# Kernel optimization log

Measured on AMD Instinct MI355X. Metric: run time of the kernel, lower is better.

Reference implementation:

```python
import jax, jax.numpy as jnp
import numpy as np

B, NQ, NK, C, H = 4, 1024, 1024, 768, 12
DH = C // H
SCALE = DH ** -0.5
EPS = 1e-5  # nn.LayerNorm default
NEG_INF = float('-inf')


def _ln(x, g, b):
    m = jnp.mean(x, axis=-1, keepdims=True)
    v = jnp.mean((x - m) ** 2, axis=-1, keepdims=True)
    return (x - m) * jax.lax.rsqrt(v + EPS) * g + b


def _heads(t):  # [B,N,C] -> [B,H,N,Dh]
    Bq, N, _ = t.shape
    return t.reshape(Bq, N, H, DH).transpose(0, 2, 1, 3)


def setup_inputs() -> dict:
    key = jax.random.key(0)
    ks = jax.random.split(key, 32)
    w = lambda k, shape: jax.random.normal(k, shape, jnp.float32) * 0.02
    g = lambda k: 1.0 + jax.random.normal(k, (C,), jnp.float32) * 0.02
    b = lambda k: jax.random.normal(k, (C,), jnp.float32) * 0.02
    inp = {
        'x': jax.random.normal(ks[0], (B, NQ, C), jnp.float32),
        'y': jax.random.normal(ks[1], (B, NK, C), jnp.float32),
        'xpos': jnp.arange(B * NQ, dtype=jnp.int32).reshape(B, NQ),
        'ypos': jnp.arange(B * NK, dtype=jnp.int32).reshape(B, NK),
        'mask': jax.random.randint(ks[2], (NQ, NK), 0, 2) > 0,
        'similarities': jax.random.normal(ks[3], (B, H, NQ, NK), jnp.float32),
        # norms
        'ln1_g': g(ks[4]), 'ln1_b': b(ks[5]),
        'ln2_g': g(ks[6]), 'ln2_b': b(ks[7]),
        'ln3_g': g(ks[8]), 'ln3_b': b(ks[9]),
        'lny_g': g(ks[10]), 'lny_b': b(ks[11]),
        # self-attn (qkv_bias=False)
        'qkv_w': w(ks[12], (3 * C, C)),
        'aproj_w': w(ks[13], (C, C)), 'aproj_b': b(ks[14]),
        # cross-attn
        'pq_w': w(ks[15], (C, C)), 'pk_w': w(ks[16], (C, C)), 'pv_w': w(ks[17], (C, C)),
        'cproj_w': w(ks[18], (C, C)), 'cproj_b': b(ks[19]),
        # mlp (hidden = 4*C)
        'fc1_w': w(ks[20], (4 * C, C)), 'fc1_b': jax.random.normal(ks[21], (4 * C,), jnp.float32) * 0.02,
        'fc2_w': w(ks[22], (C, 4 * C)), 'fc2_b': b(ks[23]),
    }
    return inp


def reference(x, y, xpos, ypos, mask, similarities,
              ln1_g, ln1_b, ln2_g, ln2_b, ln3_g, ln3_b, lny_g, lny_b,
              qkv_w, aproj_w, aproj_b,
              pq_w, pk_w, pv_w, cproj_w, cproj_b,
              fc1_w, fc1_b, fc2_w, fc2_b):
    # ---- self-attention (rope=None, dropout=0) ----
    xn = _ln(x, ln1_g, ln1_b)
    qkv = (xn @ qkv_w.T).reshape(B, NQ, 3, H, DH).transpose(2, 0, 3, 1, 4)
    q, k, v = qkv[0], qkv[1], qkv[2]                       # [B,H,Nq,Dh]
    attn = jax.nn.softmax(jnp.einsum('bhqd,bhkd->bhqk', q, k) * SCALE, axis=-1)
    sa = jnp.einsum('bhqk,bhkd->bhqd', attn, v).transpose(0, 2, 1, 3).reshape(B, NQ, C)
    x = x + sa @ aproj_w.T + aproj_b

    # ---- sparse cross-attention with similarity bias + mask ----
    y_ = _ln(y, lny_g, lny_b)
    xn2 = _ln(x, ln2_g, ln2_b)
    cq = _heads(xn2 @ pq_w.T)                              # [B,H,Nq,Dh]
    ck = _heads(y_ @ pk_w.T)                               # [B,H,Nk,Dh]
    cv = _heads(y_ @ pv_w.T)
    scores = jnp.einsum('bhqd,bhkd->bhqk', cq, ck) * SCALE
    sims_c = similarities - jnp.mean(similarities, axis=1, keepdims=True)
    scores = scores + sims_c
    scores = jnp.where(mask[None, None], scores, NEG_INF)
    cattn = jax.nn.softmax(scores, axis=-1)
    ca = jnp.einsum('bhqk,bhkd->bhqd', cattn, cv).transpose(0, 2, 1, 3).reshape(B, NQ, C)
    x = x + ca @ cproj_w.T + cproj_b

    # ---- MLP (exact GELU, as nn.GELU default) ----
    xn3 = _ln(x, ln3_g, ln3_b)
    h = jax.nn.gelu(xn3 @ fc1_w.T + fc1_b, approximate=False)
    x = x + h @ fc2_w.T + fc2_b
    return (x, y)
```

## Files before the change

### kernel.cpp

```cpp
#include <hip/hip_runtime.h>
#include <cstdint>
#include <cstddef>


typedef __bf16 bf16;
typedef __attribute__((ext_vector_type(8))) __bf16 bf16x8;
typedef __attribute__((ext_vector_type(4))) __bf16 bf16x4;
typedef __attribute__((ext_vector_type(4))) float f32x4;

typedef __attribute__((address_space(1))) void gvoid;
typedef __attribute__((address_space(3))) void lvoid;

#define DEVI static __device__ __forceinline__

DEVI void gload16(const void* g, void* l) {
  __builtin_amdgcn_global_load_lds((gvoid*)(uintptr_t)g, (lvoid*)(uintptr_t)l, 16, 0, 0);
}

DEVI f32x4 mfma_bf16(bf16x8 a, bf16x8 b, f32x4 c) {
  return __builtin_amdgcn_mfma_f32_16x16x32_bf16(a, b, c, 0, 0, 0);
}


template<int BM, int BN, bool BIAS, bool GELU, bool RES, bool OBF, bool VT>
DEVI void gemm_dev(bf16* As, bf16* Bs, int by, int bx,
                   const bf16* __restrict__ A, const bf16* __restrict__ Bt,
                   const float* __restrict__ bias, const float* __restrict__ res,
                   bf16* __restrict__ Cb, float* __restrict__ Cf,
                   bf16* __restrict__ vtOut, int vtBase, int N, int K)
{
  constexpr int WM = BM / 2, WN = BN / 2;
  constexpr int FM = WM / 16, FN = WN / 16;
  const int tid = threadIdx.x;
  const int lane = tid & 63;
  const int wv = tid >> 6;
  const int wr = wv >> 1, wc = wv & 1;
  const int l15 = lane & 15, lg = lane >> 4;
  const int bm = by * BM, bn = bx * BN;

  f32x4 acc[FM][FN];
  const f32x4 z = {0.f, 0.f, 0.f, 0.f};
  #pragma unroll
  for (int i = 0; i < FM; ++i)
    #pragma unroll
    for (int jj = 0; jj < FN; ++jj) acc[i][jj] = z;

  for (int k0 = 0; k0 < K; k0 += 64) {
    __syncthreads();
    #pragma unroll
    for (int c = tid; c < BM * 8; c += 256) {
      const int row = c >> 3, colb = (c & 7) << 4;
      gload16((const char*)A + ((size_t)(bm + row) * K + k0) * 2 + colb,
              (char*)As + (size_t)c * 16);
    }
    #pragma unroll
    for (int c = tid; c < BN * 8; c += 256) {
      const int row = c >> 3, colb = (c & 7) << 4;
      gload16((const char*)Bt + ((size_t)(bn + row) * K + k0) * 2 + colb,
              (char*)Bs + (size_t)c * 16);
    }
    __syncthreads();
    #pragma unroll
    for (int kk = 0; kk < 64; kk += 32) {
      bf16x8 af[FM], bfr[FN];
      #pragma unroll
      for (int mi = 0; mi < FM; ++mi)
        af[mi] = *(const bf16x8*)(As + (size_t)(wr * WM + mi * 16 + l15) * 64 + kk + lg * 8);
      #pragma unroll
      for (int ni = 0; ni < FN; ++ni)
        bfr[ni] = *(const bf16x8*)(Bs + (size_t)(wc * WN + ni * 16 + l15) * 64 + kk + lg * 8);
      #pragma unroll
      for (int mi = 0; mi < FM; ++mi)
        #pragma unroll
        for (int ni = 0; ni < FN; ++ni)
          acc[mi][ni] = mfma_bf16(af[mi], bfr[ni], acc[mi][ni]);
    }
  }

  #pragma unroll
  for (int mi = 0; mi < FM; ++mi) {
    const int row0 = bm + wr * WM + mi * 16 + lg * 4;
    #pragma unroll
    for (int ni = 0; ni < FN; ++ni) {
      const int col = bn + wc * WN + ni * 16 + l15;
      if constexpr (VT) {
        if (col >= vtBase) {
          const int hd = col - vtBase;
          const int bb = row0 >> 10, n0 = row0 & 1023;
          bf16x4 ov;
          #pragma unroll
          for (int r = 0; r < 4; ++r) ov[r] = (bf16)acc[mi][ni][r];
          *(bf16x4*)(vtOut + ((size_t)(bb * 768 + hd)) * 1024 + n0) = ov;
          continue;
        }
      }
      #pragma unroll
      for (int r = 0; r < 4; ++r) {
        float v = acc[mi][ni][r];
        if constexpr (BIAS) v += bias[col];
        if constexpr (GELU) v = 0.5f * v * (1.0f + erff(v * 0.70710678118654752f));
        if constexpr (RES)  v += res[(size_t)(row0 + r) * N + col];
        if constexpr (OBF)  Cb[(size_t)(row0 + r) * N + col] = (bf16)v;
        else                Cf[(size_t)(row0 + r) * N + col] = v;
      }
    }
  }
}

DEVI void lnw_dev(int row,
                  const float* __restrict__ xin, const float* __restrict__ g,
                  const float* __restrict__ be, bf16* __restrict__ out)
{
  const int lane = threadIdx.x & 63;
  const f32x4* xr = (const f32x4*)(xin + (size_t)row * 768);
  f32x4 v[3];
  #pragma unroll
  for (int j = 0; j < 3; ++j) v[j] = xr[lane + 64 * j];
  float s = 0.f;
  #pragma unroll
  for (int j = 0; j < 3; ++j) s += v[j][0] + v[j][1] + v[j][2] + v[j][3];
  #pragma unroll
  for (int o = 32; o; o >>= 1) s += __shfl_xor(s, o);
  const float mean = s * (1.0f / 768.0f);
  float q = 0.f;
  #pragma unroll
  for (int j = 0; j < 3; ++j)
    #pragma unroll
    for (int e = 0; e < 4; ++e) { const float d = v[j][e] - mean; q += d * d; }
  #pragma unroll
  for (int o = 32; o; o >>= 1) q += __shfl_xor(q, o);
  const float inv = rsqrtf(q * (1.0f / 768.0f) + 1e-5f);
  #pragma unroll
  for (int j = 0; j < 3; ++j) {
    const int c = lane + 64 * j;
    const f32x4 gv = ((const f32x4*)g)[c];
    const f32x4 bv = ((const f32x4*)be)[c];
    bf16x4 o4;
    #pragma unroll
    for (int e = 0; e < 4; ++e)
      o4[e] = (bf16)((v[j][e] - mean) * inv * gv[e] + bv[e]);
    *((bf16x4*)out + (size_t)row * 192 + c) = o4;
  }
}

DEVI void bias2_dev(int blk, int* red,
                    const float* __restrict__ sim,
                    const unsigned char* __restrict__ mask,
                    bf16* __restrict__ biasOut)
{
  const int b = blk >> 9;
  const int q0 = (blk & 511) * 2;
  const int t = threadIdx.x;
  const int k4 = t * 4;

  int ds = mask[t * 4 + 1] + mask[t * 4 + 2] + mask[t * 4 + 3];
  #pragma unroll
  for (int o = 32; o; o >>= 1) ds += __shfl_xor(ds, o);
  if ((t & 63) == 0) red[t >> 6] = ds;
  __syncthreads();
  const int msh = ((red[0] + red[1] + red[2] + red[3]) == 0) ? 2 : 0;

  const float* sb = sim + (size_t)b * 12 * 1024 * 1024;
  bf16* ob = biasOut + (size_t)b * 12 * 1024 * 1024;

  #pragma unroll
  for (int p = 0; p < 2; ++p) {
    const int q = q0 + p;
    f32x4 sv[12];
    f32x4 acc = {0.f, 0.f, 0.f, 0.f};
    #pragma unroll
    for (int h = 0; h < 12; ++h) {
      sv[h] = *(const f32x4*)(sb + ((size_t)h * 1024 + q) * 1024 + k4);
      acc += sv[h];
    }
    const f32x4 mean = acc * (1.0f / 12.0f);

    float mb[4];
    if (msh == 0) {
      const uchar4 mv = *(const uchar4*)(mask + (size_t)q * 1024 + k4);
      mb[0] = mv.x ? 0.f : -1e30f; mb[1] = mv.y ? 0.f : -1e30f;
      mb[2] = mv.z ? 0.f : -1e30f; mb[3] = mv.w ? 0.f : -1e30f;
    } else {
      const int4 mv = *(const int4*)((const int*)mask + (size_t)q * 1024 + k4);
      mb[0] = mv.x ? 0.f : -1e30f; mb[1] = mv.y ? 0.f : -1e30f;
      mb[2] = mv.z ? 0.f : -1e30f; mb[3] = mv.w ? 0.f : -1e30f;
    }

    #pragma unroll
    for (int h = 0; h < 12; ++h) {
      bf16x4 o;
      #pragma unroll
      for (int j = 0; j < 4; ++j)
        o[j] = (bf16)(sv[h][j] - mean[j] + mb[j]);
      *(bf16x4*)(ob + ((size_t)h * 1024 + q) * 1024 + k4) = o;
    }
  }
}


struct CvtArgs {
  const float* src[8];
  bf16* dst[8];
  int end[8];
};

__global__ __launch_bounds__(256)
void prep_k(CvtArgs a,
            const float* __restrict__ x, const float* __restrict__ g1,
            const float* __restrict__ b1, bf16* __restrict__ xn,
            const float* __restrict__ y, const float* __restrict__ gy,
            const float* __restrict__ by_, bf16* __restrict__ yln,
            const float* __restrict__ sim, const unsigned char* __restrict__ mask,
            bf16* __restrict__ biasA)
{
  __shared__ int red[4];
  const int f = blockIdx.x;
  const int t = threadIdx.x;
  if (f < 2304) {
    #pragma unroll
    for (int j = 0; j < 4; ++j) {
      const int i = f * 1024 + j * 256 + t;
      int s = 0;
      #pragma unroll
      for (int k = 0; k < 7; ++k) s += (i >= a.end[k]) ? 1 : 0;
      const int base = s ? a.end[s - 1] : 0;
      const int off = i - base;
      const f32x4 v = *((const f32x4*)a.src[s] + off);
      bf16x4 o;
      o[0] = (bf16)v[0]; o[1] = (bf16)v[1]; o[2] = (bf16)v[2]; o[3] = (bf16)v[3];
      *(bf16x4*)(a.dst[s] + (size_t)off * 4) = o;
    }
  } else if (f < 4352) {
    const int row = (f - 2304) * 4 + (t >> 6);
    if (row < 4096) lnw_dev(row, x, g1, b1, xn);
    else            lnw_dev(row - 4096, y, gy, by_, yln);
  } else {
    bias2_dev(f - 4352, red, sim, mask, biasA);
  }
}

__global__ __launch_bounds__(256)
void apkv_k(const bf16* __restrict__ sa, const bf16* __restrict__ w_ap,
            const float* __restrict__ apb, const float* __restrict__ x,
            float* __restrict__ x1,
            const bf16* __restrict__ yln, const bf16* __restrict__ w_pkv,
            bf16* __restrict__ ckv, bf16* __restrict__ cvtT)
{
  __shared__ bf16 As[128 * 64];
  __shared__ bf16 Bs[128 * 64];
  const int f = blockIdx.x;
  if (f < 384) {
    const int xcd = f & 7, j = f >> 3;
    const int by = xcd + 8 * (j % 8);
    const int bx = j / 8;
    gemm_dev<64,128,true,false,true,false,false>(As, Bs, by, bx,
        sa, w_ap, apb, x, nullptr, x1, nullptr, 0, 768, 768);
  } else {
    const int g = f - 384;
    const int xcd = g & 7, j = g >> 3;
    const int by = xcd + 8 * (j % 4);
    const int bx = j / 4;
    gemm_dev<128,128,false,false,false,true,true>(As, Bs, by, bx,
        yln, w_pkv, nullptr, nullptr, ckv, nullptr, cvtT, 768, 1536, 768);
  }
}

__global__ __launch_bounds__(256)
void fc2copy_k(const bf16* __restrict__ hbuf, const bf16* __restrict__ w_f2,
               const float* __restrict__ f2b, const float* __restrict__ x2,
               float* __restrict__ outp,
               const float* __restrict__ y, float* __restrict__ ycopy)
{
  __shared__ bf16 As[128 * 64];
  __shared__ bf16 Bs[128 * 64];
  const int f = blockIdx.x;
  if (f < 384) {
    const int xcd = f & 7, j = f >> 3;
    const int by = xcd + 8 * (j % 8);
    const int bx = j / 8;
    gemm_dev<64,128,true,false,true,false,false>(As, Bs, by, bx,
        hbuf, w_f2, f2b, x2, nullptr, outp, nullptr, 0, 768, 3072);
  } else {
    for (int i = (f - 384) * 256 + threadIdx.x; i < 786432; i += 512 * 256)
      ((f32x4*)ycopy)[i] = ((const f32x4*)y)[i];
  }
}

template<int BM, int BN, bool BIAS, bool GELU, bool RES, bool OBF, bool VT>
__global__ __launch_bounds__(256)
void gemm_bt(const bf16* __restrict__ A, const bf16* __restrict__ Bt,
             const float* __restrict__ bias, const float* __restrict__ res,
             bf16* __restrict__ Cb, float* __restrict__ Cf,
             bf16* __restrict__ vtOut, int vtBase,
             int nyPerXcd, int N, int K)
{
  __shared__ bf16 As[BM * 64];
  __shared__ bf16 Bs[BN * 64];
  const int f = blockIdx.x;
  const int xcd = f & 7, j = f >> 3;
  const int by = xcd + 8 * (j % nyPerXcd);
  const int bx = j / nyPerXcd;
  gemm_dev<BM,BN,BIAS,GELU,RES,OBF,VT>(As, Bs, by, bx,
      A, Bt, bias, res, Cb, Cf, vtOut, vtBase, N, K);
}

__global__ __launch_bounds__(256)
void ln_k(const float* __restrict__ xin, const float* __restrict__ g,
          const float* __restrict__ be, bf16* __restrict__ out)
{
  lnw_dev(blockIdx.x * 4 + (threadIdx.x >> 6), xin, g, be, out);
}

template<int CROSS>
__global__ __launch_bounds__(256, 3)
void fattn_k(const bf16* __restrict__ Qp, int ldq,
             const bf16* __restrict__ Kp, int ldk,
             const bf16* __restrict__ Vt,
             const bf16* __restrict__ bias,
             bf16* __restrict__ Out)
{
  __shared__ bf16 Kl[2][64 * 64];
  __shared__ bf16 Vl[2][64 * 64];
  __shared__ bf16 Pl[4][16 * 72];

  const int f = blockIdx.x;
  const int r8 = f & 7, rest = f >> 3;
  const int c6 = rest % 6, qt = rest / 6;
  const int pp = r8 + 8 * c6;
  const int b = pp / 12, hh = pp % 12;
  const int tid = threadIdx.x, lane = tid & 63, wq = tid >> 6;
  const int l15 = lane & 15, lg = lane >> 4;

  bf16x8 qreg0, qreg1;
  {
    const bf16* qsrc = Qp + (size_t)(b * 1024 + qt * 64 + wq * 16 + l15) * ldq + hh * 64 + lg * 8;
    qreg0 = *(const bf16x8*)qsrc;
    qreg1 = *(const bf16x8*)(qsrc + 32);
  }
  const char* Kbase = (const char*)(Kp + (size_t)b * 1024 * ldk + hh * 64);
  const char* Vbase = (const char*)(Vt + (size_t)(b * 12 + hh) * 64 * 1024);
  const bf16* biasRow = nullptr;
  if constexpr (CROSS)
    biasRow = bias + (((size_t)(b * 12 + hh)) * 1024 + qt * 64 + wq * 16 + l15) * 1024;

  f32x4 oacc[4];
  const f32x4 z = {0.f, 0.f, 0.f, 0.f};
  #pragma unroll
  for (int i = 0; i < 4; ++i) oacc[i] = z;
  float m_run = -1e30f, l_run = 0.f;

  char* PlW = (char*)&Pl[wq][0];
  const int swz = (l15 & 7) << 4;

  auto stage = [&](int buf, int t) {
    const int k0 = t * 64;
    #pragma unroll
    for (int jj = 0; jj < 2; ++jj) {
      const int c = jj * 256 + tid;
      const int r = c >> 3;
      const int sw = ((c & 7) ^ (r & 7)) << 4;
      gload16(Kbase + ((size_t)(k0 + r) * ldk) * 2 + sw, (char*)&Kl[buf][0] + (size_t)c * 16);
      gload16(Vbase + (size_t)r * 2048 + (size_t)k0 * 2 + sw, (char*)&Vl[buf][0] + (size_t)c * 16);
    }
  };

  stage(0, 0);
  __syncthreads();

  for (int t = 0; t < 16; ++t) {
    const int cur = t & 1;
    const int k0 = t * 64;
    if (t < 15) stage(cur ^ 1, t + 1);

    bf16x4 bv[4];
    if constexpr (CROSS) {
      const bf16* bp = biasRow + k0 + lg * 4;
      #pragma unroll
      for (int ni = 0; ni < 4; ++ni) bv[ni] = *(const bf16x4*)(bp + ni * 16);
    }

    f32x4 sacc[4];
    #pragma unroll
    for (int i = 0; i < 4; ++i) sacc[i] = z;
    #pragma unroll
    for (int ni = 0; ni < 4; ++ni) {
      const int rowb = (ni * 16 + l15) * 128;
      const bf16x8 a0 = *(const bf16x8*)((char*)&Kl[cur][0] + rowb + ((lg * 16) ^ swz));
      const bf16x8 a1 = *(const bf16x8*)((char*)&Kl[cur][0] + rowb + ((64 + lg * 16) ^ swz));
      sacc[ni] = mfma_bf16(a0, qreg0, sacc[ni]);
      sacc[ni] = mfma_bf16(a1, qreg1, sacc[ni]);
    }

    float sv[16];
    #pragma unroll
    for (int ni = 0; ni < 4; ++ni)
      #pragma unroll
      for (int r = 0; r < 4; ++r)
        sv[ni * 4 + r] = sacc[ni][r] * 0.125f;
    if constexpr (CROSS) {
      #pragma unroll
      for (int ni = 0; ni < 4; ++ni)
        #pragma unroll
        for (int r = 0; r < 4; ++r)
          sv[ni * 4 + r] += (float)bv[ni][r];
    }
    float mx = sv[0];
    #pragma unroll
    for (int jj = 1; jj < 16; ++jj) mx = fmaxf(mx, sv[jj]);
    mx = fmaxf(mx, __shfl_xor(mx, 16));
    mx = fmaxf(mx, __shfl_xor(mx, 32));
    const float mnew = fmaxf(m_run, mx);
    const float corr = __expf(m_run - mnew);
    m_run = mnew;
    float ps = 0.f;
    #pragma unroll
    for (int jj = 0; jj < 16; ++jj) { sv[jj] = __expf(sv[jj] - mnew); ps += sv[jj]; }
    l_run = l_run * corr + ps;

    #pragma unroll
    for (int ni = 0; ni < 4; ++ni) {
      bf16x4 pw;
      #pragma unroll
      for (int r = 0; r < 4; ++r) pw[r] = (bf16)sv[ni * 4 + r];
      *(bf16x4*)(PlW + l15 * 144 + ni * 32 + lg * 8) = pw;
    }
    float cr[4];
    #pragma unroll
    for (int r = 0; r < 4; ++r) cr[r] = __shfl(corr, ((lane >> 4) << 2) + r);
    #pragma unroll
    for (int nd = 0; nd < 4; ++nd)
      #pragma unroll
      for (int r = 0; r < 4; ++r) oacc[nd][r] *= cr[r];

    const bf16x8 p0 = *(const bf16x8*)(PlW + l15 * 144 + lg * 16);
    const bf16x8 p1 = *(const bf16x8*)(PlW + l15 * 144 + 64 + lg * 16);
    #pragma unroll
    for (int nd = 0; nd < 4; ++nd) {
      const int rowb = (nd * 16 + l15) * 128;
      const bf16x8 v0 = *(const bf16x8*)((char*)&Vl[cur][0] + rowb + ((lg * 16) ^ swz));
      const bf16x8 v1 = *(const bf16x8*)((char*)&Vl[cur][0] + rowb + ((64 + lg * 16) ^ swz));
      oacc[nd] = mfma_bf16(p0, v0, oacc[nd]);
      oacc[nd] = mfma_bf16(p1, v1, oacc[nd]);
    }
    __syncthreads();
  }

  float ls = l_run + __shfl_xor(l_run, 16);
  ls += __shfl_xor(ls, 32);
  const float inv = 1.0f / ls;
  float ivr[4];
  #pragma unroll
  for (int r = 0; r < 4; ++r) ivr[r] = __shfl(inv, ((lane >> 4) << 2) + r);
  bf16* ob = Out + (size_t)(b * 1024 + qt * 64 + wq * 16 + lg * 4) * 768 + hh * 64 + l15;
  #pragma unroll
  for (int r = 0; r < 4; ++r)
    #pragma unroll
    for (int nd = 0; nd < 4; ++nd)
      ob[(size_t)r * 768 + nd * 16] = (bf16)(oacc[nd][r] * ivr[r]);
}

extern "C" void kernel_launch(void* const* d_in, const int* in_sizes, int n_in,
                              void* d_out, int out_size, void* d_ws, size_t ws_size,
                              hipStream_t stream)
{
  (void)in_sizes; (void)n_in; (void)out_size; (void)ws_size;
  const float* x    = (const float*)d_in[0];
  const float* y    = (const float*)d_in[1];
  const unsigned char* mask = (const unsigned char*)d_in[4];
  const float* sim  = (const float*)d_in[5];
  const float* ln1g = (const float*)d_in[6];
  const float* ln1b = (const float*)d_in[7];
  const float* ln2g = (const float*)d_in[8];
  const float* ln2b = (const float*)d_in[9];
  const float* ln3g = (const float*)d_in[10];
  const float* ln3b = (const float*)d_in[11];
  const float* lnyg = (const float*)d_in[12];
  const float* lnyb = (const float*)d_in[13];
  const float* qkvw = (const float*)d_in[14];
  const float* apw  = (const float*)d_in[15];
  const float* apb  = (const float*)d_in[16];
  const float* pqw  = (const float*)d_in[17];
  const float* pkw  = (const float*)d_in[18];
  const float* pvw  = (const float*)d_in[19];
  const float* cpw  = (const float*)d_in[20];
  const float* cpb  = (const float*)d_in[21];
  const float* f1w  = (const float*)d_in[22];
  const float* f1b  = (const float*)d_in[23];
  const float* f2w  = (const float*)d_in[24];
  const float* f2b  = (const float*)d_in[25];

  char* ws = (char*)d_ws;
  size_t off = 0;
  auto alloc = [&](size_t bytes) -> void* {
    off = (off + 255) & ~(size_t)255;
    void* p = ws + off;
    off += bytes;
    return p;
  };
  const size_t T = 4096;
  bf16* w_qkv = (bf16*)alloc((size_t)2304 * 768 * 2);
  bf16* w_ap  = (bf16*)alloc((size_t)768 * 768 * 2);
  bf16* w_pq  = (bf16*)alloc((size_t)768 * 768 * 2);
  bf16* w_pkv = (bf16*)alloc((size_t)1536 * 768 * 2);
  bf16* w_cp  = (bf16*)alloc((size_t)768 * 768 * 2);
  bf16* w_f1  = (bf16*)alloc((size_t)3072 * 768 * 2);
  bf16* w_f2  = (bf16*)alloc((size_t)768 * 3072 * 2);
  bf16* xn    = (bf16*)alloc(T * 768 * 2);
  bf16* qkvo  = (bf16*)alloc(T * 2304 * 2);
  bf16* vt    = (bf16*)alloc((size_t)48 * 64 * 1024 * 2);
  bf16* sa    = (bf16*)alloc(T * 768 * 2);
  float* x1   = (float*)alloc(T * 768 * 4);
  bf16* yln   = (bf16*)alloc(T * 768 * 2);
  bf16* xn2   = (bf16*)alloc(T * 768 * 2);
  bf16* cqf   = (bf16*)alloc(T * 768 * 2);
  bf16* ckv   = (bf16*)alloc(T * 1536 * 2);
  bf16* cvtT  = (bf16*)alloc((size_t)48 * 64 * 1024 * 2);
  bf16* biasA = (bf16*)alloc((size_t)4 * 12 * 1024 * 1024 * 2);
  bf16* ca    = (bf16*)alloc(T * 768 * 2);
  float* x2   = (float*)alloc(T * 768 * 4);
  bf16* xn3   = (bf16*)alloc(T * 768 * 2);
  bf16* hbuf  = (bf16*)alloc(T * 3072 * 2);

  CvtArgs a;
  {
    const float* srcs[8] = {qkvw, apw, pqw, pkw, pvw, cpw, f1w, f2w};
    bf16* dsts[8] = {w_qkv, w_ap, w_pq, w_pkv, w_pkv + 768 * 768, w_cp, w_f1, w_f2};
    const int n4s[8] = {442368, 147456, 147456, 147456, 147456, 147456, 589824, 589824};
    int cum = 0;
    for (int j = 0; j < 8; ++j) {
      a.src[j] = srcs[j]; a.dst[j] = dsts[j];
      cum += n4s[j]; a.end[j] = cum;
    }
  }

  prep_k<<<6400, 256, 0, stream>>>(a, x, ln1g, ln1b, xn, y, lnyg, lnyb, yln,
                                   sim, mask, biasA);

  gemm_bt<128,128,false,false,false,true,true><<<576, 256, 0, stream>>>(
      xn, w_qkv, nullptr, nullptr, qkvo, nullptr, vt, 1536, 4, 2304, 768);

  fattn_k<0><<<768, 256, 0, stream>>>(
      qkvo, 2304, qkvo + 768, 2304, vt, nullptr, sa);

  apkv_k<<<768, 256, 0, stream>>>(sa, w_ap, apb, x, x1, yln, w_pkv, ckv, cvtT);

  ln_k<<<1024, 256, 0, stream>>>(x1, ln2g, ln2b, xn2);

  gemm_bt<64,128,false,false,false,true,false><<<384, 256, 0, stream>>>(
      xn2, w_pq, nullptr, nullptr, cqf, nullptr, nullptr, 0, 8, 768, 768);

  fattn_k<1><<<768, 256, 0, stream>>>(
      cqf, 768, ckv, 1536, cvtT, biasA, ca);

  gemm_bt<64,128,true,false,true,false,false><<<384, 256, 0, stream>>>(
      ca, w_cp, cpb, x1, nullptr, x2, nullptr, 0, 8, 768, 768);

  ln_k<<<1024, 256, 0, stream>>>(x2, ln3g, ln3b, xn3);

  gemm_bt<128,128,true,true,false,true,false><<<768, 256, 0, stream>>>(
      xn3, w_f1, f1b, nullptr, hbuf, nullptr, nullptr, 0, 4, 3072, 768);

  fc2copy_k<<<896, 256, 0, stream>>>(
      hbuf, w_f2, f2b, x2, (float*)d_out, y, (float*)d_out + 3145728);
}
```

Before: 380.2 us.

## Split bias precompute into its own kernel and store bias query-major

Moves the similarity-centering and mask bias computation out of the fused prep kernel into a dedicated kernel. Each block handles one (batch, query) row and stages the 12 head rows in shared memory before computing the head mean. The bias buffer layout changes from [B,H,Q,K] to [B,Q,H,K] so each block writes one contiguous 24 KB region, and the cross-attention kernel's bias indexing is updated to match. The cost is an extra kernel launch, high LDS use per block that limits occupancy, and a different access stride when cross-attention reads the bias.

```diff
diff --git a/kernel.cpp b/kernel.cpp
--- a/kernel.cpp
+++ b/kernel.cpp
@@ -143,60 +143,6 @@
   }
 }
 
-DEVI void bias2_dev(int blk, int* red,
-                    const float* __restrict__ sim,
-                    const unsigned char* __restrict__ mask,
-                    bf16* __restrict__ biasOut)
-{
-  const int b = blk >> 9;
-  const int q0 = (blk & 511) * 2;
-  const int t = threadIdx.x;
-  const int k4 = t * 4;
-
-  int ds = mask[t * 4 + 1] + mask[t * 4 + 2] + mask[t * 4 + 3];
-  #pragma unroll
-  for (int o = 32; o; o >>= 1) ds += __shfl_xor(ds, o);
-  if ((t & 63) == 0) red[t >> 6] = ds;
-  __syncthreads();
-  const int msh = ((red[0] + red[1] + red[2] + red[3]) == 0) ? 2 : 0;
-
-  const float* sb = sim + (size_t)b * 12 * 1024 * 1024;
-  bf16* ob = biasOut + (size_t)b * 12 * 1024 * 1024;
-
-  #pragma unroll
-  for (int p = 0; p < 2; ++p) {
-    const int q = q0 + p;
-    f32x4 sv[12];
-    f32x4 acc = {0.f, 0.f, 0.f, 0.f};
-    #pragma unroll
-    for (int h = 0; h < 12; ++h) {
-      sv[h] = *(const f32x4*)(sb + ((size_t)h * 1024 + q) * 1024 + k4);
-      acc += sv[h];
-    }
-    const f32x4 mean = acc * (1.0f / 12.0f);
-
-    float mb[4];
-    if (msh == 0) {
-      const uchar4 mv = *(const uchar4*)(mask + (size_t)q * 1024 + k4);
-      mb[0] = mv.x ? 0.f : -1e30f; mb[1] = mv.y ? 0.f : -1e30f;
-      mb[2] = mv.z ? 0.f : -1e30f; mb[3] = mv.w ? 0.f : -1e30f;
-    } else {
-      const int4 mv = *(const int4*)((const int*)mask + (size_t)q * 1024 + k4);
-      mb[0] = mv.x ? 0.f : -1e30f; mb[1] = mv.y ? 0.f : -1e30f;
-      mb[2] = mv.z ? 0.f : -1e30f; mb[3] = mv.w ? 0.f : -1e30f;
-    }
-
-    #pragma unroll
-    for (int h = 0; h < 12; ++h) {
-      bf16x4 o;
-      #pragma unroll
-      for (int j = 0; j < 4; ++j)
-        o[j] = (bf16)(sv[h][j] - mean[j] + mb[j]);
-      *(bf16x4*)(ob + ((size_t)h * 1024 + q) * 1024 + k4) = o;
-    }
-  }
-}
-
 
 struct CvtArgs {
   const float* src[8];
@@ -209,11 +155,8 @@
             const float* __restrict__ x, const float* __restrict__ g1,
             const float* __restrict__ b1, bf16* __restrict__ xn,
             const float* __restrict__ y, const float* __restrict__ gy,
-            const float* __restrict__ by_, bf16* __restrict__ yln,
-            const float* __restrict__ sim, const unsigned char* __restrict__ mask,
-            bf16* __restrict__ biasA)
-{
-  __shared__ int red[4];
+            const float* __restrict__ by_, bf16* __restrict__ yln)
+{
   const int f = blockIdx.x;
   const int t = threadIdx.x;
   if (f < 2304) {
@@ -230,12 +173,69 @@
       o[0] = (bf16)v[0]; o[1] = (bf16)v[1]; o[2] = (bf16)v[2]; o[3] = (bf16)v[3];
       *(bf16x4*)(a.dst[s] + (size_t)off * 4) = o;
     }
-  } else if (f < 4352) {
+  } else {
     const int row = (f - 2304) * 4 + (t >> 6);
     if (row < 4096) lnw_dev(row, x, g1, b1, xn);
     else            lnw_dev(row - 4096, y, gy, by_, yln);
+  }
+}
+
+__global__ __launch_bounds__(256)
+void bias_k(const float* __restrict__ sim,
+            const unsigned char* __restrict__ mask,
+            bf16* __restrict__ biasOut)
+{
+  __shared__ float S[12 * 1032];
+  __shared__ int red[4];
+  const int blk = blockIdx.x;
+  const int b = blk >> 10, q = blk & 1023;
+  const int t = threadIdx.x, lane = t & 63, w = t >> 6;
+
+  int ds = mask[t * 4 + 1] + mask[t * 4 + 2] + mask[t * 4 + 3];
+  #pragma unroll
+  for (int o = 32; o; o >>= 1) ds += __shfl_xor(ds, o);
+  if (lane == 0) red[w] = ds;
+
+  const float* sb = sim + (size_t)b * 12 * 1048576;
+  #pragma unroll
+  for (int i = 0; i < 3; ++i) {
+    const int h = w + i * 4;
+    const f32x4* src = (const f32x4*)(sb + ((size_t)h * 1024 + q) * 1024);
+    #pragma unroll
+    for (int jj = 0; jj < 4; ++jj) {
+      const int c = lane + 64 * jj;
+      *(f32x4*)(&S[h * 1032 + c * 4]) = src[c];
+    }
+  }
+  __syncthreads();
+  const int msh = ((red[0] + red[1] + red[2] + red[3]) == 0) ? 2 : 0;
+
+  const int k4 = t * 4;
+  float mb[4];
+  if (msh == 0) {
+    const uchar4 mv = *(const uchar4*)(mask + (size_t)q * 1024 + k4);
+    mb[0] = mv.x ? 0.f : -1e30f; mb[1] = mv.y ? 0.f : -1e30f;
+    mb[2] = mv.z ? 0.f : -1e30f; mb[3] = mv.w ? 0.f : -1e30f;
   } else {
-    bias2_dev(f - 4352, red, sim, mask, biasA);
+    const int4 mv = *(const int4*)((const int*)mask + (size_t)q * 1024 + k4);
+    mb[0] = mv.x ? 0.f : -1e30f; mb[1] = mv.y ? 0.f : -1e30f;
+    mb[2] = mv.z ? 0.f : -1e30f; mb[3] = mv.w ? 0.f : -1e30f;
+  }
+
+  f32x4 acc = {0.f, 0.f, 0.f, 0.f};
+  #pragma unroll
+  for (int h = 0; h < 12; ++h) acc += *(const f32x4*)(&S[h * 1032 + k4]);
+  const f32x4 mean = acc * (1.0f / 12.0f);
+
+  bf16* ob = biasOut + (size_t)(b * 1024 + q) * 12 * 1024;
+  #pragma unroll
+  for (int h = 0; h < 12; ++h) {
+    const f32x4 sv = *(const f32x4*)(&S[h * 1032 + k4]);
+    bf16x4 o;
+    #pragma unroll
+    for (int j = 0; j < 4; ++j)
+      o[j] = (bf16)(sv[j] - mean[j] + mb[j]);
+    *(bf16x4*)(ob + h * 1024 + k4) = o;
   }
 }
 
@@ -341,7 +341,7 @@
   const char* Vbase = (const char*)(Vt + (size_t)(b * 12 + hh) * 64 * 1024);
   const bf16* biasRow = nullptr;
   if constexpr (CROSS)
-    biasRow = bias + (((size_t)(b * 12 + hh)) * 1024 + qt * 64 + wq * 16 + l15) * 1024;
+    biasRow = bias + ((size_t)(b * 1024 + qt * 64 + wq * 16 + l15) * 12 + hh) * 1024;
 
   f32x4 oacc[4];
   const f32x4 z = {0.f, 0.f, 0.f, 0.f};
@@ -515,7 +515,7 @@
   bf16* cqf   = (bf16*)alloc(T * 768 * 2);
   bf16* ckv   = (bf16*)alloc(T * 1536 * 2);
   bf16* cvtT  = (bf16*)alloc((size_t)48 * 64 * 1024 * 2);
-  bf16* biasA = (bf16*)alloc((size_t)4 * 12 * 1024 * 1024 * 2);
+  bf16* biasA = (bf16*)alloc((size_t)4 * 1024 * 12 * 1024 * 2);
   bf16* ca    = (bf16*)alloc(T * 768 * 2);
   float* x2   = (float*)alloc(T * 768 * 4);
   bf16* xn3   = (bf16*)alloc(T * 768 * 2);
@@ -533,8 +533,9 @@
     }
   }
 
-  prep_k<<<6400, 256, 0, stream>>>(a, x, ln1g, ln1b, xn, y, lnyg, lnyb, yln,
-                                   sim, mask, biasA);
+  prep_k<<<4352, 256, 0, stream>>>(a, x, ln1g, ln1b, xn, y, lnyg, lnyb, yln);
+
+  bias_k<<<4096, 256, 0, stream>>>(sim, mask, biasA);
 
   gemm_bt<128,128,false,false,false,true,true><<<576, 256, 0, stream>>>(
       xn, w_qkv, nullptr, nullptr, qkvo, nullptr, vt, 1536, 4, 2304, 768);
```

Measured after the change: 388.0 us. 1.02x slower.
